# Performance work log

Hardware: AMD Instinct MI355X
Metric: run time of the kernel (lower is better)

The kernel has to match this reference:

```python
import jax, jax.numpy as jnp
import numpy as np

B, T, D, N, K, H = 2, 2048, 2048, 16, 8, 128
WIN = 1024                      # sliding_window_size
SOFT_CAP = 50.0                 # attn_logits_soft_cap
SCALAR = 0.08838834764831845    # query_pre_attn_scalar = head_dim**-0.5
K_MASK = -2.3819763e+38
ROPE_BASE = 10000.0
ROPE_SCALE = 1.0


def apply_rope(x, positions):
    # x: [B, T, heads, H]; positions: [B, T]
    head_dim = x.shape[-1]
    half = head_dim // 2
    timescale = ROPE_BASE ** (2.0 * jnp.arange(half, dtype=jnp.float32) / head_dim)
    sinusoid = positions[..., None].astype(jnp.float32) / timescale / ROPE_SCALE  # [B,T,half]
    sin = jnp.sin(sinusoid)[:, :, None, :]
    cos = jnp.cos(sinusoid)[:, :, None, :]
    first, second = jnp.split(x, 2, axis=-1)
    return jnp.concatenate(
        [first * cos - second * sin, second * cos + first * sin], axis=-1
    ).astype(x.dtype)


def setup_inputs() -> dict:
    key = jax.random.key(0)
    k0, k1, k2, k3 = jax.random.split(key, 4)
    x = jax.random.normal(k0, (B, T, D), jnp.float32)
    wq = jax.random.normal(k1, (N, D, H), jnp.float32) * (D ** -0.5)
    wkv = jax.random.normal(k2, (2, K, D, H), jnp.float32) * (D ** -0.5)
    wo = jax.random.normal(k3, (N, H, D), jnp.float32) * ((N * H) ** -0.5)
    segment_pos = jnp.broadcast_to(jnp.arange(T, dtype=jnp.int32), (B, T))
    attn_mask = jnp.broadcast_to(jnp.tril(jnp.ones((T, T), dtype=bool)), (B, T, T))  # causal
    return {"x": x, "wq": wq, "wkv": wkv, "wo": wo,
            "segment_pos": segment_pos, "attn_mask": attn_mask}


def reference(x, wq, wkv, wo, segment_pos, attn_mask):
    # --- projections ---
    q = jnp.einsum('BTD,NDH->BTNH', x, wq)          # [B,T,N,H]
    kv = jnp.einsum('BTD,CKDH->CBTKH', x, wkv)      # [2,B,T,K,H]
    k_proj, v_proj = kv[0], kv[1]
    # --- RoPE + query scaling ---
    q = apply_rope(q, segment_pos) * SCALAR
    k_proj = apply_rope(k_proj, segment_pos)
    # --- GQA logits ---
    G = N // K
    qg = q.reshape(B, T, K, G, H)
    logits = jnp.einsum('BTKGH,BSKH->BTKGS', qg, k_proj).reshape(B, T, N, T)
    # --- soft cap ---
    logits = jnp.tanh(logits / SOFT_CAP) * SOFT_CAP
    # --- sliding-window mask combined with causal attn_mask ---
    all_ones = jnp.ones(attn_mask.shape, dtype=attn_mask.dtype)
    sliding_mask = jnp.triu(all_ones, -WIN + 1) * jnp.tril(all_ones, WIN - 1)
    mask = sliding_mask * attn_mask                  # [B,T,S]
    padded_logits = jnp.where(mask[:, :, None, :], logits, K_MASK)
    probs = jax.nn.softmax(padded_logits, axis=-1).astype(k_proj.dtype)
    # --- GQA weighted values ---
    encoded = jnp.einsum('BTKGS,BSKH->BTKGH',
                         probs.reshape(B, T, K, G, T), v_proj).reshape(B, T, N, H)
    # --- output projection ---
    return jnp.einsum('BTNH,NHD->BTD', encoded, wo)
```

## Files before the change

kernel.cpp:

```cpp
#include <hip/hip_runtime.h>
#include <stdint.h>

#define BDIM 2
#define TDIM 2048
#define DDIM 2048
#define NHEADS 16
#define KVH 8
#define HDIM 128
#define WINSZ 1024
#define BT (BDIM*TDIM)
#define NHD (NHEADS*HDIM)
#define QKVC 4096

typedef unsigned short u16;
typedef __attribute__((ext_vector_type(8))) short bf16x8;
typedef __attribute__((ext_vector_type(4))) float f32x4;

__device__ __forceinline__ u16 f2bf(float f) {
  union { float f; unsigned u; } v; v.f = f;
  unsigned r = v.u + 0x7FFFu + ((v.u >> 16) & 1u);
  return (u16)(r >> 16);
}
__device__ __forceinline__ float bf2f(u16 u) {
  union { unsigned u; float f; } v; v.u = ((unsigned)u) << 16;
  return v.f;
}

__device__ __forceinline__ void gl_lds16(const u16* g, u16* l) {
  __builtin_amdgcn_global_load_lds((const __attribute__((address_space(1))) void*)g,
                                   (__attribute__((address_space(3))) void*)l, 16, 0, 0);
}

__global__ void k_rope_table(const int* __restrict__ seg, float2* __restrict__ tab) {
  int t = blockIdx.x, b = blockIdx.y, i = threadIdx.x;
  int pos = seg[b*TDIM + t];
  float inv_ts = exp2f(-(float)i * (13.287712379549449f/64.0f));
  float ang = (float)pos * inv_ts;
  tab[(size_t)(b*TDIM + t)*64 + i] = make_float2(cosf(ang), sinf(ang));
}

__global__ void k_cvt_bf16(const float* __restrict__ x, u16* __restrict__ y, int n4) {
  int i = blockIdx.x*blockDim.x + threadIdx.x;
  if (i < n4) {
    float4 v = ((const float4*)x)[i];
    ushort4 o;
    o.x = f2bf(v.x); o.y = f2bf(v.y); o.z = f2bf(v.z); o.w = f2bf(v.w);
    ((ushort4*)y)[i] = o;
  }
}

template<int MODE>
__global__ void k_build_wt(const float* __restrict__ s0p, const float* __restrict__ s1p,
                           u16* __restrict__ dst) {
  __shared__ float tl[32][33];
  int tx = threadIdx.x, ty = threadIdx.y;
  int r0 = blockIdx.x*32, c0 = blockIdx.y*32;
  #pragma unroll
  for (int i = 0; i < 4; i++) {
    int r = r0 + tx, c = c0 + ty + i*8;
    const float* sp; size_t off;
    if (MODE == 0) {
      if (r < 2048) { sp = s0p; off = (size_t)(r >> 7)*262144u + (size_t)(r & 127); }
      else { int j = r - 2048; sp = s1p; off = (size_t)((j >> 10)*8 + ((j >> 7) & 7))*262144u + (size_t)(j & 127); }
      off += (size_t)c * 128u;
    } else {
      sp = s0p; off = (size_t)c * 2048u + (size_t)r;
    }
    tl[tx][ty + i*8] = sp[off];
  }
  __syncthreads();
  #pragma unroll
  for (int i = 0; i < 4; i++) {
    int rl = ty + i*8;
    dst[(size_t)(r0 + rl)*2048u + (size_t)(c0 + tx)] = f2bf(tl[rl][tx]);
  }
}

template<int F32OUT>
__global__ __launch_bounds__(256) void k_gemm(const u16* __restrict__ A, const u16* __restrict__ Bt,
                                              void* __restrict__ Cout, int M, int Ncols, int Kdim, int ldc) {
  __shared__ u16 As[128*64];
  __shared__ u16 Bs[128*64];
  const int tid = threadIdx.x, lane = tid & 63, wave = tid >> 6;
  const int m0 = blockIdx.x * 128, n0 = blockIdx.y * 128;
  const int wr = wave >> 1, wc = wave & 1;
  const int l15 = lane & 15, lg = lane >> 4;
  f32x4 acc[4][4] = {};
  for (int kt = 0; kt < Kdim; kt += 64) {
    __syncthreads();
    #pragma unroll
    for (int i = 0; i < 4; i++) {
      int chb = i*256 + wave*64;
      int ch = chb + lane;
      int r = ch >> 3, cc = ch & 7;
      gl_lds16(A + (size_t)(m0 + r)*Kdim + kt + cc*8, As + chb*8);
      gl_lds16(Bt + (size_t)(n0 + r)*Kdim + kt + cc*8, Bs + chb*8);
    }
    __syncthreads();
    #pragma unroll
    for (int ks = 0; ks < 2; ks++) {
      bf16x8 af[4], bf[4];
      int kk = ks*32 + lg*8;
      #pragma unroll
      for (int mt = 0; mt < 4; mt++) af[mt] = *(const bf16x8*)(As + (wr*64 + mt*16 + l15)*64 + kk);
      #pragma unroll
      for (int nt = 0; nt < 4; nt++) bf[nt] = *(const bf16x8*)(Bs + (wc*64 + nt*16 + l15)*64 + kk);
      #pragma unroll
      for (int mt = 0; mt < 4; mt++)
        #pragma unroll
        for (int nt = 0; nt < 4; nt++)
          acc[mt][nt] = __builtin_amdgcn_mfma_f32_16x16x32_bf16(af[mt], bf[nt], acc[mt][nt], 0, 0, 0);
    }
  }
  #pragma unroll
  for (int mt = 0; mt < 4; mt++) {
    int row = m0 + wr*64 + mt*16 + lg*4;
    #pragma unroll
    for (int nt = 0; nt < 4; nt++) {
      int col = n0 + wc*64 + nt*16 + l15;
      #pragma unroll
      for (int j = 0; j < 4; j++) {
        if (F32OUT) ((float*)Cout)[(size_t)(row + j)*ldc + col] = acc[mt][nt][j];
        else        ((u16*)Cout)[(size_t)(row + j)*ldc + col] = f2bf(acc[mt][nt][j]);
      }
    }
  }
}

template<int F32OUT>
__global__ __launch_bounds__(512, 2) void k_gemm8(const u16* __restrict__ A, const u16* __restrict__ Bt,
                                                  void* __restrict__ Cout, int M, int Ncols, int Kdim, int ldc) {
  __shared__ u16 As[2][256*64];
  __shared__ u16 Bs[2][256*64];
  const int tid = threadIdx.x, lane = tid & 63, wave = tid >> 6;
  const int l15 = lane & 15, lg = lane >> 4;
  const int wm = wave >> 2, wn = wave & 3;
  const int gx = M >> 8, gy = Ncols >> 8;
  const int nwg = gx * gy;
  int bid = blockIdx.x;
  int q = nwg >> 3, r = nwg & 7;
  int xcd = bid & 7, idx = bid >> 3;
  int wg = (xcd < r ? xcd*(q+1) : r*(q+1) + (xcd - r)*q) + idx;
  const int m0 = (wg % gx) * 256, n0 = (wg / gx) * 256;

  const int st_r = tid >> 3;
  const int st_c = (tid & 7) ^ (st_r & 7);

  const u16* Ag = A + (size_t)(m0 + st_r)*Kdim + st_c*8;
  const u16* Bg = Bt + (size_t)(n0 + st_r)*Kdim + st_c*8;

  auto stage = [&](int t, int h) {
    int buf = t & 1;
    if (h < 2) {
      const u16* g = Bg + (size_t)(h*128)*Kdim + t*64;
      u16* d = &Bs[buf][h*8192 + wave*512];
      gl_lds16(g, d);
      gl_lds16(g + (size_t)64*Kdim, d + 4096);
    } else {
      int hh = h - 2;
      const u16* g = Ag + (size_t)(hh*128)*Kdim + t*64;
      u16* d = &As[buf][hh*8192 + wave*512];
      gl_lds16(g, d);
      gl_lds16(g + (size_t)64*Kdim, d + 4096);
    }
  };

  const int aBase = (wm*128 + l15) * 128;
  const int bBase = (wn*64 + l15) * 128;
  const int kx0 = ((lg) ^ (l15 & 7)) << 4;
  const int kx1 = ((4 + lg) ^ (l15 & 7)) << 4;

  f32x4 acc[8][4] = {};
  bf16x8 af[4][2], bfr[4][2];

  stage(0,0); stage(0,1); stage(0,2); stage(0,3);
  asm volatile("s_waitcnt vmcnt(4)" ::: "memory");
  stage(1,0); stage(1,1); stage(1,2);
  asm volatile("s_waitcnt vmcnt(6)" ::: "memory");
  __builtin_amdgcn_s_barrier();

  const int NT = Kdim >> 6;

#define MFMA_Q(MS, NS)                                                          \
  { _Pragma("unroll") for (int mf = 0; mf < 4; mf++)                            \
    _Pragma("unroll") for (int nf = 0; nf < 2; nf++) {                          \
      acc[(MS)+mf][(NS)+nf] = __builtin_amdgcn_mfma_f32_16x16x32_bf16(af[mf][0], bfr[(NS)+nf][0], acc[(MS)+mf][(NS)+nf], 0, 0, 0); \
      acc[(MS)+mf][(NS)+nf] = __builtin_amdgcn_mfma_f32_16x16x32_bf16(af[mf][1], bfr[(NS)+nf][1], acc[(MS)+mf][(NS)+nf], 0, 0, 0); \
  } }

  for (int t = 0; t < NT; ++t) {
    const int cur = t & 1;
    const char* Ab = (const char*)&As[cur][0];
    const char* Bb = (const char*)&Bs[cur][0];
    #pragma unroll
    for (int mf = 0; mf < 4; mf++) {
      af[mf][0] = *(const bf16x8*)(Ab + aBase + mf*2048 + kx0);
      af[mf][1] = *(const bf16x8*)(Ab + aBase + mf*2048 + kx1);
    }
    #pragma unroll
    for (int nf = 0; nf < 2; nf++) {
      bfr[nf][0] = *(const bf16x8*)(Bb + bBase + nf*2048 + kx0);
      bfr[nf][1] = *(const bf16x8*)(Bb + bBase + nf*2048 + kx1);
    }
    if (t + 1 < NT) stage(t+1, 3);
    asm volatile("s_waitcnt lgkmcnt(8)" ::: "memory");
    __builtin_amdgcn_s_barrier();
    asm volatile("s_waitcnt lgkmcnt(0)" ::: "memory");
    __builtin_amdgcn_sched_barrier(0);
    __builtin_amdgcn_s_setprio(1);
    MFMA_Q(0, 0)
    __builtin_amdgcn_s_setprio(0);
    __builtin_amdgcn_s_barrier();
    #pragma unroll
    for (int nf = 2; nf < 4; nf++) {
      bfr[nf][0] = *(const bf16x8*)(Bb + bBase + nf*2048 + kx0);
      bfr[nf][1] = *(const bf16x8*)(Bb + bBase + nf*2048 + kx1);
    }
    __builtin_amdgcn_s_barrier();
    asm volatile("s_waitcnt lgkmcnt(0)" ::: "memory");
    __builtin_amdgcn_sched_barrier(0);
    __builtin_amdgcn_s_setprio(1);
    MFMA_Q(0, 2)
    __builtin_amdgcn_s_setprio(0);
    __builtin_amdgcn_s_barrier();
    #pragma unroll
    for (int mf = 0; mf < 4; mf++) {
      af[mf][0] = *(const bf16x8*)(Ab + aBase + 8192 + mf*2048 + kx0);
      af[mf][1] = *(const bf16x8*)(Ab + aBase + 8192 + mf*2048 + kx1);
    }
    if (t + 2 < NT) { stage(t+2, 0); stage(t+2, 1); }
    __builtin_amdgcn_s_barrier();
    asm volatile("s_waitcnt lgkmcnt(0)" ::: "memory");
    __builtin_amdgcn_sched_barrier(0);
    __builtin_amdgcn_s_setprio(1);
    MFMA_Q(4, 2)
    __builtin_amdgcn_s_setprio(0);
    __builtin_amdgcn_s_barrier();
    if (t + 2 < NT) {
      stage(t+2, 2);
      asm volatile("s_waitcnt vmcnt(6)" ::: "memory");
    } else if (t + 1 < NT) {
      asm volatile("s_waitcnt vmcnt(0)" ::: "memory");
    }
    __builtin_amdgcn_s_barrier();
    __builtin_amdgcn_s_setprio(1);
    MFMA_Q(4, 0)
    __builtin_amdgcn_s_setprio(0);
    __builtin_amdgcn_s_barrier();
  }
#undef MFMA_Q

  #pragma unroll
  for (int mf = 0; mf < 8; mf++) {
    int row = m0 + wm*128 + mf*16 + lg*4;
    #pragma unroll
    for (int nf = 0; nf < 4; nf++) {
      int col = n0 + wn*64 + nf*16 + l15;
      #pragma unroll
      for (int j = 0; j < 4; j++) {
        if (F32OUT) ((float*)Cout)[(size_t)(row + j)*ldc + col] = acc[mf][nf][j];
        else        ((u16*)Cout)[(size_t)(row + j)*ldc + col] = f2bf(acc[mf][nf][j]);
      }
    }
  }
}

__global__ void k_rope(u16* __restrict__ qkv, const float2* __restrict__ tab) {
  int p = blockIdx.x*blockDim.x + threadIdx.x;
  int t = blockIdx.y, b = blockIdx.z;
  int col, i; float sc;
  if (p < 1024) { int n = p >> 6; i = p & 63; col = n*128 + i; sc = 0.08838834764831845f; }
  else          { int p2 = p - 1024; int kh = p2 >> 6; i = p2 & 63; col = 2048 + kh*128 + i; sc = 1.0f; }
  float2 cs = tab[(size_t)(b*TDIM + t)*64 + i];
  u16* row = qkv + (size_t)(b*TDIM + t)*QKVC;
  float f = bf2f(row[col]), s = bf2f(row[col + 64]);
  float o1 = (f*cs.x - s*cs.y) * sc;
  float o2 = (s*cs.x + f*cs.y) * sc;
  row[col] = f2bf(o1); row[col + 64] = f2bf(o2);
}

__global__ void k_build_vt(const u16* __restrict__ qkv, u16* __restrict__ vT) {
  __shared__ u16 tl[32][33];
  int tx = threadIdx.x, ty = threadIdx.y;
  int t0 = blockIdx.x*32, h0 = blockIdx.y*32, bk = blockIdx.z;
  const u16* src = qkv + (size_t)(bk >> 3)*TDIM*QKVC + 3072 + (bk & 7)*HDIM;
  #pragma unroll
  for (int i = 0; i < 4; i++)
    tl[ty + i*8][tx] = src[(size_t)(t0 + ty + i*8)*QKVC + h0 + tx];
  __syncthreads();
  u16* dst = vT + (size_t)bk*HDIM*TDIM;
  #pragma unroll
  for (int i = 0; i < 4; i++)
    dst[(size_t)(h0 + ty + i*8)*TDIM + t0 + tx] = tl[tx][ty + i*8];
}

__device__ __forceinline__ void stage_tiles(const u16* __restrict__ kg, const u16* __restrict__ vg,
                                            u16* ldsK, u16* ldsV, int tid) {
  const int w = tid >> 6;
  const int rK = tid >> 4, cK = tid & 15;
  u16* dK = ldsK + w*512;
  gl_lds16(kg + (size_t)rK*QKVC + ((cK ^ (rK & 15)) << 3), dK);
  gl_lds16(kg + (size_t)(rK + 32)*QKVC + ((cK ^ ((rK + 32) & 15)) << 3), dK + 4096);
  const int rV = tid >> 3, cV = tid & 7;
  u16* dV = ldsV + w*512;
  gl_lds16(vg + (size_t)rV*TDIM + ((cV ^ (rV & 7)) << 3), dV);
  gl_lds16(vg + (size_t)(rV + 64)*TDIM + ((cV ^ ((rV + 64) & 7)) << 3), dV + 4096);
}

__global__ __launch_bounds__(512, 4) void k_attn(const u16* __restrict__ qkv, const u16* __restrict__ vT,
                                                 u16* __restrict__ enc) {
  __shared__ u16 Kb[2][64*128];
  __shared__ u16 Vb[2][128*64];
  __shared__ u16 Pl[8][16*64];
  const int tid = threadIdx.x;
  const int lane = tid & 63, wave = tid >> 6;
  const int l15 = lane & 15, lg = lane >> 4;
  const int wg = blockIdx.x;
  const int lin = (wg & 7)*64 + (wg >> 3);
  const int qt = lin & 31, kvh = (lin >> 5) & 7, b = lin >> 8;
  const int n = kvh*2 + (wave >> 2);
  const int t0 = qt * 64;
  const int lo_row = t0 + (wave & 3)*16, hi_row = lo_row + 15;

  bf16x8 qf[4];
  {
    const u16* qb = qkv + (size_t)(b*TDIM + lo_row + l15)*QKVC + n*HDIM + lg*8;
    #pragma unroll
    for (int ks = 0; ks < 4; ks++) qf[ks] = *(const bf16x8*)(qb + ks*32);
  }
  float l_r[4] = {0.f, 0.f, 0.f, 0.f};
  f32x4 o[8] = {};

  const u16* kgb = qkv + (size_t)(b*TDIM)*QKVC + 2048 + kvh*HDIM;
  const u16* vgb = vT + (size_t)(b*KVH + kvh)*HDIM*TDIM;

  const float C1 = -1.3333333333e-4f;
  const float C2 = 2.1333333333e-8f;
  const float LOG2E = 1.4426950408889634f;
  const float BIAS = -72.13475204444817f;

  const int s_begin = (t0 >= 1024) ? (t0 - 1024) : 0;
  stage_tiles(kgb + (size_t)s_begin*QKVC, vgb + s_begin, Kb[0], Vb[0], tid);
  int cur = 0;
  for (int s0 = s_begin; s0 <= t0; s0 += 64) {
    if (s0 + 64 <= t0) {
      stage_tiles(kgb + (size_t)(s0 + 64)*QKVC, vgb + (s0 + 64), Kb[cur ^ 1], Vb[cur ^ 1], tid);
      asm volatile("s_waitcnt vmcnt(4)" ::: "memory");
    } else {
      asm volatile("s_waitcnt vmcnt(0)" ::: "memory");
    }
    __builtin_amdgcn_s_barrier();
    __builtin_amdgcn_sched_barrier(0);

    const u16* Kc = Kb[cur];
    const u16* Vc = Vb[cur];
    f32x4 sc4[4];
    #pragma unroll
    for (int c = 0; c < 4; c++) {
      const int cLo = s0 + c*16;
      bool anyLive = (cLo <= hi_row) && (cLo + 15 >= lo_row - (WINSZ - 1));
      bool full    = (cLo + 15 <= lo_row) && (cLo >= hi_row - (WINSZ - 1));
      f32x4 a = {0.f, 0.f, 0.f, 0.f};
      if (anyLive) {
        int krow = c*16 + l15;
        __builtin_amdgcn_s_setprio(1);
        #pragma unroll
        for (int ks = 0; ks < 4; ks++) {
          bf16x8 kf = *(const bf16x8*)(Kc + krow*128 + (((ks*4 + lg) ^ l15) << 3));
          a = __builtin_amdgcn_mfma_f32_16x16x32_bf16(qf[ks], kf, a, 0, 0, 0);
        }
        __builtin_amdgcn_s_setprio(0);
        if (full) {
          #pragma unroll
          for (int j = 0; j < 4; j++) {
            float z = a[j];
            float u = z*z;
            float w = z * __builtin_fmaf(u, __builtin_fmaf(u, C2, C1), 1.0f);
            float p = exp2f(__builtin_fmaf(w, LOG2E, BIAS));
            a[j] = p;
            l_r[j] += p;
          }
        } else {
          #pragma unroll
          for (int j = 0; j < 4; j++) {
            int scol = cLo + l15;
            int trow = lo_row + lg*4 + j;
            float z = a[j];
            float u = z*z;
            float w = z * __builtin_fmaf(u, __builtin_fmaf(u, C2, C1), 1.0f);
            float p = exp2f(__builtin_fmaf(w, LOG2E, BIAS));
            bool ok = (scol <= trow) && (scol >= trow - (WINSZ - 1));
            p = ok ? p : 0.f;
            a[j] = p;
            l_r[j] += p;
          }
        }
      }
      sc4[c] = a;
    }
    #pragma unroll
    for (int c = 0; c < 4; c++)
      #pragma unroll
      for (int j = 0; j < 4; j++) {
        int prow = lg*4 + j, pcol = c*16 + l15;
        int off = prow*128 + pcol*2; off ^= (prow & 7) << 4;
        *(u16*)((char*)(&Pl[wave][0]) + off) = f2bf(sc4[c][j]);
      }
    __builtin_amdgcn_s_setprio(1);
    #pragma unroll
    for (int ks = 0; ks < 2; ks++) {
      int roff = l15*128 + ks*64 + lg*16; roff ^= (l15 & 7) << 4;
      bf16x8 pf = *(const bf16x8*)((char*)(&Pl[wave][0]) + roff);
      #pragma unroll
      for (int ct = 0; ct < 8; ct++) {
        int vrow = ct*16 + l15;
        bf16x8 vf = *(const bf16x8*)(Vc + vrow*64 + (((ks*4 + lg) ^ (l15 & 7)) << 3));
        o[ct] = __builtin_amdgcn_mfma_f32_16x16x32_bf16(pf, vf, o[ct], 0, 0, 0);
      }
    }
    __builtin_amdgcn_s_setprio(0);
    __builtin_amdgcn_s_barrier();
    cur ^= 1;
  }
  #pragma unroll
  for (int j = 0; j < 4; j++) {
    float l = l_r[j];
    #pragma unroll
    for (int d = 1; d < 16; d <<= 1) l += __shfl_xor(l, d);
    float inv = __fdividef(1.f, l);
    int row = lo_row + lg*4 + j;
    u16* eb = enc + (size_t)(b*TDIM + row)*NHD + n*HDIM;
    #pragma unroll
    for (int ct = 0; ct < 8; ct++)
      eb[ct*16 + l15] = f2bf(o[ct][j] * inv);
  }
}

extern "C" void kernel_launch(void* const* d_in, const int* in_sizes, int n_in,
                              void* d_out, int out_size, void* d_ws, size_t ws_size,
                              hipStream_t stream) {
  const float* x   = (const float*)d_in[0];
  const float* wq  = (const float*)d_in[1];
  const float* wkv = (const float*)d_in[2];
  const float* wo  = (const float*)d_in[3];
  const int*   seg = (const int*)d_in[4];
  float* out = (float*)d_out;

  char* ws = (char*)d_ws;
  u16*    x_bf   = (u16*)(ws);
  u16*    wt_qkv = (u16*)(ws + (16u << 20));
  u16*    qkv    = (u16*)(ws + (32u << 20));
  u16*    vT     = (u16*)(ws + (64u << 20));
  u16*    enc    = (u16*)(ws + (72u << 20));
  u16*    wo_t   = (u16*)(ws + (88u << 20));
  float2* tab    = (float2*)(ws + (96u << 20));

  k_rope_table<<<dim3(TDIM, BDIM), 64, 0, stream>>>(seg, tab);
  k_cvt_bf16<<<(BT*DDIM/4 + 255)/256, 256, 0, stream>>>(x, x_bf, BT*DDIM/4);
  k_build_wt<0><<<dim3(128, 64), dim3(32, 8), 0, stream>>>(wq, wkv, wt_qkv);
  k_build_wt<1><<<dim3(64, 64), dim3(32, 8), 0, stream>>>(wo, nullptr, wo_t);
  k_gemm8<0><<<dim3((BT/256)*(QKVC/256)), 512, 0, stream>>>(x_bf, wt_qkv, qkv, BT, QKVC, DDIM, QKVC);
  k_rope<<<dim3(6, TDIM, BDIM), 256, 0, stream>>>(qkv, tab);
  k_build_vt<<<dim3(TDIM/32, HDIM/32, BDIM*KVH), dim3(32, 8), 0, stream>>>(qkv, vT);
  k_attn<<<dim3(512), 512, 0, stream>>>(qkv, vT, enc);
  k_gemm<1><<<dim3(BT/128, DDIM/128), 256, 0, stream>>>(enc, wo_t, out, BT, DDIM, NHD, DDIM);
}
```

Baseline: 226.6 us.

## Reorder GEMM MFMA quadrants, vectorize RoPE, sum softmax rows via MFMA

The QKV GEMM main loop is rearranged so the first-quadrant fragments for the next K-tile are prefetched from LDS at the end of the current iteration, and the MFMA quadrant order and global staging points are shuffled. RoPE is rewritten as one block per token that does 8-wide vector loads and stores. In attention, the tanh polynomial is folded into the log2e multiply, and the per-lane row-sum plus its shuffle reduction is replaced by an extra MFMA against a ones vector. These changes aim to cut LDS latency stalls, memory transactions and ALU work, but the extra MFMA per step and the new schedule could add pressure elsewhere.

```diff
diff --git a/kernel.cpp b/kernel.cpp
--- a/kernel.cpp
+++ b/kernel.cpp
@@ -174,10 +174,23 @@
   bf16x8 af[4][2], bfr[4][2];
 
   stage(0,0); stage(0,1); stage(0,2); stage(0,3);
-  asm volatile("s_waitcnt vmcnt(4)" ::: "memory");
   stage(1,0); stage(1,1); stage(1,2);
   asm volatile("s_waitcnt vmcnt(6)" ::: "memory");
   __builtin_amdgcn_s_barrier();
+  {
+    const char* Ab = (const char*)&As[0][0];
+    const char* Bb = (const char*)&Bs[0][0];
+    #pragma unroll
+    for (int mf = 0; mf < 4; mf++) {
+      af[mf][0] = *(const bf16x8*)(Ab + aBase + mf*2048 + kx0);
+      af[mf][1] = *(const bf16x8*)(Ab + aBase + mf*2048 + kx1);
+    }
+    #pragma unroll
+    for (int nf = 0; nf < 2; nf++) {
+      bfr[nf][0] = *(const bf16x8*)(Bb + bBase + nf*2048 + kx0);
+      bfr[nf][1] = *(const bf16x8*)(Bb + bBase + nf*2048 + kx1);
+    }
+  }
 
   const int NT = Kdim >> 6;
 
@@ -190,20 +203,10 @@
 
   for (int t = 0; t < NT; ++t) {
     const int cur = t & 1;
-    const char* Ab = (const char*)&As[cur][0];
-    const char* Bb = (const char*)&Bs[cur][0];
-    #pragma unroll
-    for (int mf = 0; mf < 4; mf++) {
-      af[mf][0] = *(const bf16x8*)(Ab + aBase + mf*2048 + kx0);
-      af[mf][1] = *(const bf16x8*)(Ab + aBase + mf*2048 + kx1);
-    }
-    #pragma unroll
-    for (int nf = 0; nf < 2; nf++) {
-      bfr[nf][0] = *(const bf16x8*)(Bb + bBase + nf*2048 + kx0);
-      bfr[nf][1] = *(const bf16x8*)(Bb + bBase + nf*2048 + kx1);
-    }
-    if (t + 1 < NT) stage(t+1, 3);
-    asm volatile("s_waitcnt lgkmcnt(8)" ::: "memory");
+    const char* Ab  = (const char*)&As[cur][0];
+    const char* Bb  = (const char*)&Bs[cur][0];
+    const char* Abn = (const char*)&As[cur ^ 1][0];
+    const char* Bbn = (const char*)&Bs[cur ^ 1][0];
     __builtin_amdgcn_s_barrier();
     asm volatile("s_waitcnt lgkmcnt(0)" ::: "memory");
     __builtin_amdgcn_sched_barrier(0);
@@ -216,6 +219,7 @@
       bfr[nf][0] = *(const bf16x8*)(Bb + bBase + nf*2048 + kx0);
       bfr[nf][1] = *(const bf16x8*)(Bb + bBase + nf*2048 + kx1);
     }
+    if (t + 1 < NT) stage(t+1, 3);
     __builtin_amdgcn_s_barrier();
     asm volatile("s_waitcnt lgkmcnt(0)" ::: "memory");
     __builtin_amdgcn_sched_barrier(0);
@@ -228,6 +232,13 @@
       af[mf][0] = *(const bf16x8*)(Ab + aBase + 8192 + mf*2048 + kx0);
       af[mf][1] = *(const bf16x8*)(Ab + aBase + 8192 + mf*2048 + kx1);
     }
+    __builtin_amdgcn_s_barrier();
+    asm volatile("s_waitcnt lgkmcnt(0)" ::: "memory");
+    __builtin_amdgcn_sched_barrier(0);
+    __builtin_amdgcn_s_setprio(1);
+    MFMA_Q(4, 0)
+    __builtin_amdgcn_s_setprio(0);
+    __builtin_amdgcn_s_barrier();
     if (t + 2 < NT) { stage(t+2, 0); stage(t+2, 1); }
     __builtin_amdgcn_s_barrier();
     asm volatile("s_waitcnt lgkmcnt(0)" ::: "memory");
@@ -242,11 +253,18 @@
     } else if (t + 1 < NT) {
       asm volatile("s_waitcnt vmcnt(0)" ::: "memory");
     }
-    __builtin_amdgcn_s_barrier();
-    __builtin_amdgcn_s_setprio(1);
-    MFMA_Q(4, 0)
-    __builtin_amdgcn_s_setprio(0);
-    __builtin_amdgcn_s_barrier();
+    if (t + 1 < NT) {
+      #pragma unroll
+      for (int mf = 0; mf < 4; mf++) {
+        af[mf][0] = *(const bf16x8*)(Abn + aBase + mf*2048 + kx0);
+        af[mf][1] = *(const bf16x8*)(Abn + aBase + mf*2048 + kx1);
+      }
+      #pragma unroll
+      for (int nf = 0; nf < 2; nf++) {
+        bfr[nf][0] = *(const bf16x8*)(Bbn + bBase + nf*2048 + kx0);
+        bfr[nf][1] = *(const bf16x8*)(Bbn + bBase + nf*2048 + kx1);
+      }
+    }
   }
 #undef MFMA_Q
 
@@ -265,18 +283,29 @@
   }
 }
 
-__global__ void k_rope(u16* __restrict__ qkv, const float2* __restrict__ tab) {
-  int p = blockIdx.x*blockDim.x + threadIdx.x;
-  int t = blockIdx.y, b = blockIdx.z;
-  int col, i; float sc;
-  if (p < 1024) { int n = p >> 6; i = p & 63; col = n*128 + i; sc = 0.08838834764831845f; }
-  else          { int p2 = p - 1024; int kh = p2 >> 6; i = p2 & 63; col = 2048 + kh*128 + i; sc = 1.0f; }
-  float2 cs = tab[(size_t)(b*TDIM + t)*64 + i];
-  u16* row = qkv + (size_t)(b*TDIM + t)*QKVC;
-  float f = bf2f(row[col]), s = bf2f(row[col + 64]);
-  float o1 = (f*cs.x - s*cs.y) * sc;
-  float o2 = (s*cs.x + f*cs.y) * sc;
-  row[col] = f2bf(o1); row[col + 64] = f2bf(o2);
+__global__ void k_rope2(u16* __restrict__ qkv, const float2* __restrict__ tab) {
+  const int tid = threadIdx.x;
+  const int bt = blockIdx.x;
+  const int h = tid >> 3, g = tid & 7;
+  const int col0 = (h < 16 ? h*128 : 2048 + (h - 16)*128) + g*8;
+  const float sc = (h < 16) ? 0.08838834764831845f : 1.0f;
+  u16* row = qkv + (size_t)bt*QKVC;
+  bf16x8 v1 = *(const bf16x8*)(row + col0);
+  bf16x8 v2 = *(const bf16x8*)(row + col0 + 64);
+  const float4* t4 = (const float4*)(tab + (size_t)bt*64 + g*8);
+  bf16x8 r1, r2;
+  #pragma unroll
+  for (int i = 0; i < 4; i++) {
+    float4 cs2 = t4[i];
+    float f0 = bf2f((u16)v1[2*i]),   s0 = bf2f((u16)v2[2*i]);
+    float f1 = bf2f((u16)v1[2*i+1]), s1 = bf2f((u16)v2[2*i+1]);
+    r1[2*i]   = (short)f2bf((f0*cs2.x - s0*cs2.y)*sc);
+    r2[2*i]   = (short)f2bf((s0*cs2.x + f0*cs2.y)*sc);
+    r1[2*i+1] = (short)f2bf((f1*cs2.z - s1*cs2.w)*sc);
+    r2[2*i+1] = (short)f2bf((s1*cs2.z + f1*cs2.w)*sc);
+  }
+  *(bf16x8*)(row + col0) = r1;
+  *(bf16x8*)(row + col0 + 64) = r2;
 }
 
 __global__ void k_build_vt(const u16* __restrict__ qkv, u16* __restrict__ vT) {
@@ -328,15 +357,17 @@
     #pragma unroll
     for (int ks = 0; ks < 4; ks++) qf[ks] = *(const bf16x8*)(qb + ks*32);
   }
-  float l_r[4] = {0.f, 0.f, 0.f, 0.f};
   f32x4 o[8] = {};
+  f32x4 o_l = {};
+  const short one_bf = (short)0x3F80;
+  const bf16x8 ones = {one_bf, one_bf, one_bf, one_bf, one_bf, one_bf, one_bf, one_bf};
 
   const u16* kgb = qkv + (size_t)(b*TDIM)*QKVC + 2048 + kvh*HDIM;
   const u16* vgb = vT + (size_t)(b*KVH + kvh)*HDIM*TDIM;
 
-  const float C1 = -1.3333333333e-4f;
-  const float C2 = 2.1333333333e-8f;
-  const float LOG2E = 1.4426950408889634f;
+  const float L0 = 1.4426950408889634f;
+  const float L1 = -1.9235933878519513e-4f;
+  const float L2 = 3.0777094205631089e-8f;
   const float BIAS = -72.13475204444817f;
 
   const int s_begin = (t0 >= 1024) ? (t0 - 1024) : 0;
@@ -375,10 +406,8 @@
           for (int j = 0; j < 4; j++) {
             float z = a[j];
             float u = z*z;
-            float w = z * __builtin_fmaf(u, __builtin_fmaf(u, C2, C1), 1.0f);
-            float p = exp2f(__builtin_fmaf(w, LOG2E, BIAS));
-            a[j] = p;
-            l_r[j] += p;
+            float tt = __builtin_fmaf(u, __builtin_fmaf(u, L2, L1), L0);
+            a[j] = exp2f(__builtin_fmaf(z, tt, BIAS));
           }
         } else {
           #pragma unroll
@@ -387,12 +416,10 @@
             int trow = lo_row + lg*4 + j;
             float z = a[j];
             float u = z*z;
-            float w = z * __builtin_fmaf(u, __builtin_fmaf(u, C2, C1), 1.0f);
-            float p = exp2f(__builtin_fmaf(w, LOG2E, BIAS));
+            float tt = __builtin_fmaf(u, __builtin_fmaf(u, L2, L1), L0);
+            float p = exp2f(__builtin_fmaf(z, tt, BIAS));
             bool ok = (scol <= trow) && (scol >= trow - (WINSZ - 1));
-            p = ok ? p : 0.f;
-            a[j] = p;
-            l_r[j] += p;
+            a[j] = ok ? p : 0.f;
           }
         }
       }
@@ -411,6 +438,7 @@
     for (int ks = 0; ks < 2; ks++) {
       int roff = l15*128 + ks*64 + lg*16; roff ^= (l15 & 7) << 4;
       bf16x8 pf = *(const bf16x8*)((char*)(&Pl[wave][0]) + roff);
+      o_l = __builtin_amdgcn_mfma_f32_16x16x32_bf16(pf, ones, o_l, 0, 0, 0);
       #pragma unroll
       for (int ct = 0; ct < 8; ct++) {
         int vrow = ct*16 + l15;
@@ -424,10 +452,7 @@
   }
   #pragma unroll
   for (int j = 0; j < 4; j++) {
-    float l = l_r[j];
-    #pragma unroll
-    for (int d = 1; d < 16; d <<= 1) l += __shfl_xor(l, d);
-    float inv = __fdividef(1.f, l);
+    float inv = __fdividef(1.f, o_l[j]);
     int row = lo_row + lg*4 + j;
     u16* eb = enc + (size_t)(b*TDIM + row)*NHD + n*HDIM;
     #pragma unroll
@@ -460,7 +485,7 @@
   k_build_wt<0><<<dim3(128, 64), dim3(32, 8), 0, stream>>>(wq, wkv, wt_qkv);
   k_build_wt<1><<<dim3(64, 64), dim3(32, 8), 0, stream>>>(wo, nullptr, wo_t);
   k_gemm8<0><<<dim3((BT/256)*(QKVC/256)), 512, 0, stream>>>(x_bf, wt_qkv, qkv, BT, QKVC, DDIM, QKVC);
-  k_rope<<<dim3(6, TDIM, BDIM), 256, 0, stream>>>(qkv, tab);
+  k_rope2<<<dim3(BT), 192, 0, stream>>>(qkv, tab);
   k_build_vt<<<dim3(TDIM/32, HDIM/32, BDIM*KVH), dim3(32, 8), 0, stream>>>(qkv, vT);
   k_attn<<<dim3(512), 512, 0, stream>>>(qkv, vT, enc);
   k_gemm<1><<<dim3(BT/128, DDIM/128), 256, 0, stream>>>(enc, wo_t, out, BT, DDIM, NHD, DDIM);
```

Result: no change. 224.9 us (-0.7%).
